# Optimization experiments

Measured on AMD Instinct MI355X. Metric: run time of the kernel, lower is better.

## Reference

```python
import jax, jax.numpy as jnp
import numpy as np
from jax import lax

B, DIM, H, W = 2, 128, 192, 192
GS = [16, 32, 32, 48]          # group ratios [1,2,2,3]/8 of DIM
HID = int(DIM * 2.66)          # 340, Restormer-style hidden width


def _pool_mat(n_in, n_out):
    # torch AdaptiveAvgPool as an explicit linear map [n_out, n_in]
    P = np.zeros((n_out, n_in), np.float32)
    for o in range(n_out):
        s = (o * n_in) // n_out
        e = ((o + 1) * n_in + n_out - 1) // n_out
        P[o, s:e] = 1.0 / (e - s)
    return jnp.asarray(P)


def _ln(t, w, b):
    # WithBias LayerNorm over the channel dim of NCHW (== LN over last dim of b(hw)c)
    mu = t.mean(1, keepdims=True)
    var = ((t - mu) ** 2).mean(1, keepdims=True)
    return (t - mu) / jnp.sqrt(var + 1e-5) * w[None, :, None, None] + b[None, :, None, None]


def _c1x1(t, w):
    return jnp.einsum('oc,bchw->bohw', w, t)


def _dw3(t, w):
    return lax.conv_general_dilated(t, w, (1, 1), 'SAME',
                                    dimension_numbers=('NCHW', 'OIHW', 'NCHW'),
                                    feature_group_count=t.shape[1])


def _c1d(t, w, b):
    return jnp.einsum('oc,bcl->bol', w, t) + b[None, :, None]


def _gelu(t):
    return jax.nn.gelu(t, approximate=False)


def _forward(x, qv_cache, ln1_w, ln1_b, ln2_w, ln2_b, temperature, w_qkv, w_qkv_dw, w_proj,
             intra_down_w, intra_down_b, intra_up_w, intra_up_b, intra_gate_w, intra_gate_b,
             inter0_cw_w, inter0_cw_b, inter0_g_w, inter0_g_b,
             inter1_cw_w, inter1_cw_b, inter1_g_w, inter1_g_b,
             inter2_cw_w, inter2_cw_b, inter2_g_w, inter2_g_b,
             inter3_cw_w, inter3_cw_b, inter3_g_w, inter3_g_b,
             ffn_in_w, ffn_dw_w, ffn_out_w):
    b, c, h, w_ = x.shape
    hw = h * w_
    inter_p = [(inter0_cw_w, inter0_cw_b, inter0_g_w, inter0_g_b),
               (inter1_cw_w, inter1_cw_b, inter1_g_w, inter1_g_b),
               (inter2_cw_w, inter2_cw_b, inter2_g_w, inter2_g_b),
               (inter3_cw_w, inter3_cw_b, inter3_g_w, inter3_g_b)]
    # ---- attention branch ----
    xn = _ln(x, ln1_w, ln1_b)
    qkv = _dw3(_c1x1(xn, w_qkv), w_qkv_dw)
    q, k, v = jnp.split(qkv, 3, axis=1)
    q = q.reshape(b, c, hw); k = k.reshape(b, c, hw); v = v.reshape(b, c, hw)
    # correlation-based channel re-grouping (torch.corrcoef on batch-mean of q)
    cf = q.mean(0)                                   # [C, HW]
    xm = cf - cf.mean(1, keepdims=True)
    cov = xm @ xm.T
    dsd = jnp.sqrt(jnp.diagonal(cov))
    corr = cov / (dsd[:, None] * dsd[None, :])
    idx = jnp.argsort(-corr.mean(1))                 # descending mean similarity
    q = q[:, idx]; k = k[:, idx]; v = v[:, idx]
    atts, tmpc, outs = [], [], []
    start = 0
    for i, g in enumerate(GS):
        qg = q[:, start:start + g]; kg = k[:, start:start + g]; vg = v[:, start:start + g]
        start += g
        qn = qg / jnp.maximum(jnp.linalg.norm(qg, axis=-1, keepdims=True), 1e-12)
        kn = kg / jnp.maximum(jnp.linalg.norm(kg, axis=-1, keepdims=True), 1e-12)
        att = jax.nn.softmax(jnp.einsum('bcl,bdl->bcd', qn, kn) * temperature[i, 0, 0], axis=-1)
        tmpc.append(lax.stop_gradient(qn) + lax.stop_gradient(kn))
        # Inter_CacheModulation: adaptive-pool cache to [g,g], FiLM + gated conv1d
        cw_w, cw_b, g_w, g_b = inter_p[i]
        P = _pool_mat(c, g)
        aligned = jnp.einsum('oi,bij,pj->bop', P, qv_cache, P)    # [1, g, g]
        scale, shift = jnp.split(_c1d(aligned + att, cw_w, cw_b), 2, axis=1)
        x1p = att * scale + shift
        att = x1p * _gelu(_c1d(x1p, g_w, g_b)) + att
        atts.append(att)
        outs.append(jnp.einsum('bcd,bdl->bcl', att, vg))
    # CalculateCurrentLayerCache: resize each group's batch-mean attn to [C,C].
    # Original does (u * c_i) // dim with c_i == dim, i.e. elementwise floor.
    acc = jnp.zeros((1, c, c), x.dtype)
    for a in atts:
        m = lax.stop_gradient(a).mean(0, keepdims=True)[:, None]  # [1,1,g,g]
        u = jax.image.resize(m, (1, 1, c, c), method='bilinear')
        acc = acc + jnp.floor(u)[:, 0]
    qv_new = qv_cache * 0.9 + acc * 0.1
    out_all = jnp.concatenate(outs, axis=1)          # [B, C, HW]
    tmp_all = jnp.concatenate(tmpc, axis=1)
    # Intra_CacheModulation
    s = tmp_all + out_all
    gated = _gelu(_c1d(s, intra_gate_w, intra_gate_b)) * s
    out_all = _c1d(_c1d(gated, intra_down_w, intra_down_b), intra_up_w, intra_up_b) + out_all
    x1 = x + _c1x1(out_all.reshape(b, c, h, w_), w_proj)
    # ---- gated-dconv FFN ----
    xn2 = _ln(x1, ln2_w, ln2_b)
    y1, y2 = jnp.split(_dw3(_c1x1(xn2, ffn_in_w), ffn_dw_w), 2, axis=1)
    out = x1 + _c1x1(_gelu(y1) * y2, ffn_out_w)
    return out, qv_new


def setup_inputs() -> dict:
    key = jax.random.key(0)
    ks = jax.random.split(key, 40)
    def w(i, shape, s=0.02):
        return jax.random.normal(ks[i], shape, jnp.float32) * s
    p = {}
    p['x'] = jax.random.normal(ks[0], (B, DIM, H, W), jnp.float32)
    p['qv_cache'] = jax.random.uniform(ks[1], (1, DIM, DIM), jnp.float32)
    p['ln1_w'] = jnp.ones((DIM,), jnp.float32); p['ln1_b'] = jnp.zeros((DIM,), jnp.float32)
    p['ln2_w'] = jnp.ones((DIM,), jnp.float32); p['ln2_b'] = jnp.zeros((DIM,), jnp.float32)
    p['temperature'] = jnp.ones((4, 1, 1), jnp.float32)
    p['w_qkv'] = w(2, (3 * DIM, DIM))
    p['w_qkv_dw'] = w(3, (3 * DIM, 1, 3, 3))
    p['w_proj'] = w(4, (DIM, DIM))
    p['intra_down_w'] = w(5, (DIM // 2, DIM)); p['intra_down_b'] = jnp.zeros((DIM // 2,), jnp.float32)
    p['intra_up_w'] = w(6, (DIM, DIM // 2)); p['intra_up_b'] = jnp.zeros((DIM,), jnp.float32)
    p['intra_gate_w'] = w(7, (DIM, DIM)); p['intra_gate_b'] = jnp.zeros((DIM,), jnp.float32)
    for i, g in enumerate(GS):
        p[f'inter{i}_cw_w'] = w(8 + 2 * i, (2 * g, g))
        p[f'inter{i}_cw_b'] = jnp.zeros((2 * g,), jnp.float32)
        p[f'inter{i}_g_w'] = w(9 + 2 * i, (g, g))
        p[f'inter{i}_g_b'] = jnp.zeros((g,), jnp.float32)
    p['ffn_in_w'] = w(20, (2 * HID, DIM))
    p['ffn_dw_w'] = w(21, (2 * HID, 1, 3, 3))
    p['ffn_out_w'] = w(22, (DIM, HID))
    return p


def reference(x, qv_cache, ln1_w, ln1_b, ln2_w, ln2_b, temperature, w_qkv, w_qkv_dw, w_proj,
              intra_down_w, intra_down_b, intra_up_w, intra_up_b, intra_gate_w, intra_gate_b,
              inter0_cw_w, inter0_cw_b, inter0_g_w, inter0_g_b,
              inter1_cw_w, inter1_cw_b, inter1_g_w, inter1_g_b,
              inter2_cw_w, inter2_cw_b, inter2_g_w, inter2_g_b,
              inter3_cw_w, inter3_cw_b, inter3_g_w, inter3_g_b,
              ffn_in_w, ffn_dw_w, ffn_out_w):
    return _forward(x, qv_cache, ln1_w, ln1_b, ln2_w, ln2_b, temperature, w_qkv, w_qkv_dw, w_proj,
                    intra_down_w, intra_down_b, intra_up_w, intra_up_b, intra_gate_w, intra_gate_b,
                    inter0_cw_w, inter0_cw_b, inter0_g_w, inter0_g_b,
                    inter1_cw_w, inter1_cw_b, inter1_g_w, inter1_g_b,
                    inter2_cw_w, inter2_cw_b, inter2_g_w, inter2_g_b,
                    inter3_cw_w, inter3_cw_b, inter3_g_w, inter3_g_b,
                    ffn_in_w, ffn_dw_w, ffn_out_w)
```

## Files before the change

### kernel.cpp

```cpp
#include <hip/hip_runtime.h>
#include <math.h>

#define TPB 256

constexpr int BN_  = 2;
constexpr int CDIM = 128;
constexpr int HH   = 192;
constexpr int WW   = 192;
constexpr int HWc  = HH * WW;
constexpr int C3   = 384;
constexpr int HID  = 340;
constexpr int NL2  = 288;
constexpr int CH2  = HWc / NL2;
constexpr int CV   = 288;

typedef unsigned short bf16_t;
typedef __attribute__((ext_vector_type(8))) __bf16 bf16x8;
typedef __attribute__((ext_vector_type(4))) float f32x4;

__device__ __forceinline__ float b2f(bf16_t v) {
  unsigned u = ((unsigned)v) << 16;
  return __uint_as_float(u);
}
__device__ __forceinline__ bf16_t f2b(float f) {
  unsigned u = __float_as_uint(f);
  unsigned r = (u + 0x7FFFu + ((u >> 16) & 1u)) >> 16;
  return (bf16_t)r;
}
__device__ __forceinline__ float ldf(const float* p) { return *p; }
__device__ __forceinline__ float ldf(const bf16_t* p) { return b2f(*p); }
__device__ __forceinline__ void stf(float* p, float v) { *p = v; }
__device__ __forceinline__ void stf(bf16_t* p, float v) { *p = f2b(v); }

__device__ __forceinline__ void ldv4(const float* p, float* v) {
  float4 t = *(const float4*)p;
  v[0] = t.x; v[1] = t.y; v[2] = t.z; v[3] = t.w;
}
__device__ __forceinline__ void ldv4(const bf16_t* p, float* v) {
  ushort4 t = *(const ushort4*)p;
  v[0] = b2f(t.x); v[1] = b2f(t.y); v[2] = b2f(t.z); v[3] = b2f(t.w);
}
__device__ __forceinline__ void stv4(float* p, const float* v) {
  float4 t; t.x = v[0]; t.y = v[1]; t.z = v[2]; t.w = v[3];
  *(float4*)p = t;
}
__device__ __forceinline__ void stv4(bf16_t* p, const float* v) {
  ushort4 t; t.x = f2b(v[0]); t.y = f2b(v[1]); t.z = f2b(v[2]); t.w = f2b(v[3]);
  *(ushort4*)p = t;
}

__device__ __forceinline__ float gelu_f(float x) {
  return 0.5f * x * (1.0f + erff(x * 0.7071067811865475f));
}

__device__ __forceinline__ void unpack8(uint4 v, float* rv) {
  unsigned wv[4] = {v.x, v.y, v.z, v.w};
#pragma unroll
  for (int j = 0; j < 8; ++j)
    rv[j + 1] = b2f((bf16_t)((wv[j >> 1] >> ((j & 1) * 16)) & 0xFFFFu));
}
__device__ __forceinline__ uint4 pack8(const float* a) {
  uint4 o;
  unsigned w[4];
#pragma unroll
  for (int p = 0; p < 4; ++p) {
    unsigned lo = f2b(a[2 * p]), hi = f2b(a[2 * p + 1]);
    w[p] = lo | (hi << 16);
  }
  o.x = w[0]; o.y = w[1]; o.z = w[2]; o.w = w[3];
  return o;
}
__device__ __forceinline__ float sumsq8(uint4 v) {
  unsigned w[4] = {v.x, v.y, v.z, v.w};
  float s = 0.f;
#pragma unroll
  for (int j = 0; j < 8; ++j) {
    float t = b2f((bf16_t)((w[j >> 1] >> ((j & 1) * 16)) & 0xFFFFu));
    s += t * t;
  }
  return s;
}

__device__ __forceinline__ void dwrow(const bf16_t* rp, int w8, float* rv) {
  unpack8(*(const uint4*)rp, rv);
  rv[0] = (w8 > 0) ? b2f(rp[-1]) : 0.f;
  rv[9] = (w8 + 8 < WW) ? b2f(rp[8]) : 0.f;
}

__device__ __constant__ int dGSZ[4]   = {16, 32, 32, 48};
__device__ __constant__ int dGST[4]   = {0, 16, 48, 80};
__device__ __constant__ int dAOFF[4]  = {0, 256, 1280, 2304};
__device__ __constant__ int dABASE[4] = {0, 512, 2560, 4608};

constexpr size_t oATTRAW  = 0;
constexpr size_t oATTS2   = 65536;
constexpr size_t oWB      = 131072;
constexpr size_t oQKP2    = 602112;
constexpr size_t oMUPC    = 897024;
constexpr size_t oATTS    = 1327104;
constexpr size_t oNORMQ   = 1363968;
constexpr size_t oNORMK   = 1364992;
constexpr size_t oIDX     = 1366016;
constexpr size_t oMU      = 1366528;
constexpr size_t oCOV     = 1367040;
constexpr size_t oQKV     = 1572864;
constexpr size_t oXN      = 58195968;
constexpr size_t oOUTALL  = 77070336;
constexpr size_t oSBUF    = 95944704;
constexpr size_t WS_NEED  = 114819072;
constexpr size_t oCHUNK1  = oOUTALL;
constexpr size_t oCOVPART = oOUTALL;
constexpr size_t oCOVP2   = oSBUF;
constexpr size_t oQKPART  = oXN;
constexpr size_t oGATED   = oQKV;
constexpr size_t oDBUF    = oQKV + 18874368;
constexpr size_t oY0C     = oOUTALL;
constexpr size_t oZ       = oQKV;
constexpr size_t oX1B     = oXN;

constexpr int eWQ   = 0;
constexpr int eGATE = 49152;
constexpr int eDOWN = 65536;
constexpr int eUP   = 73728;
constexpr int ePROJ = 81920;
constexpr int eFFI  = 98304;
constexpr int eFFO  = 185344;
constexpr int eTOT  = 234496;

__global__ __launch_bounds__(TPB) void k_wcvt(const float* __restrict__ wq,
                                              const float* __restrict__ gate,
                                              const float* __restrict__ down,
                                              const float* __restrict__ up,
                                              const float* __restrict__ proj,
                                              const float* __restrict__ ffi,
                                              const float* __restrict__ ffo,
                                              bf16_t* __restrict__ wb) {
  int t = blockIdx.x * TPB + threadIdx.x;
  if (t >= eTOT) return;
  int u = t;
  if (u < 49152) { wb[eWQ + u] = f2b(wq[u]); return; }
  u -= 49152;
  if (u < 16384) { wb[eGATE + u] = f2b(gate[u]); return; }
  u -= 16384;
  if (u < 8192)  { wb[eDOWN + u] = f2b(down[u]); return; }
  u -= 8192;
  if (u < 8192)  { wb[eUP + u] = f2b(up[u]); return; }
  u -= 8192;
  if (u < 16384) { wb[ePROJ + u] = f2b(proj[u]); return; }
  u -= 16384;
  if (u < 87040) { wb[eFFI + u] = f2b(ffi[u]); return; }
  u -= 87040;
  {
    int o = u / 384, k = u - o * 384;
    wb[eFFO + u] = (k < HID) ? f2b(ffo[o * HID + k]) : (bf16_t)0;
  }
}

template <typename TI>
__global__ __launch_bounds__(TPB) void k_ln(const TI* __restrict__ x,
                                            const float* __restrict__ w,
                                            const float* __restrict__ bias,
                                            bf16_t* __restrict__ out) {
  int t = blockIdx.x * TPB + threadIdx.x;
  if (t >= BN_ * HWc) return;
  int b = t / HWc, l = t - b * HWc;
  const TI* xb = x + (size_t)b * CDIM * HWc + l;
  float s = 0.f, s2 = 0.f;
#pragma unroll 4
  for (int c = 0; c < CDIM; ++c) { float v = ldf(&xb[(size_t)c * HWc]); s += v; s2 += v * v; }
  float mu  = s * (1.f / CDIM);
  float var = s2 * (1.f / CDIM) - mu * mu;
  float inv = 1.f / sqrtf(var + 1e-5f);
  bf16_t* ob = out + (size_t)b * CDIM * HWc + l;
#pragma unroll 4
  for (int c = 0; c < CDIM; ++c)
    stf(&ob[(size_t)c * HWc], (ldf(&xb[(size_t)c * HWc]) - mu) * inv * w[c] + bias[c]);
}

template <typename TO, typename TA, int KT, int EPI>
__global__ __launch_bounds__(TPB) void k_mgA(const bf16_t* __restrict__ W,
                                             const bf16_t* __restrict__ W2, int osplit,
                                             const float* __restrict__ bias,
                                             const bf16_t* __restrict__ in,
                                             const TA* __restrict__ aux,
                                             TO* __restrict__ out, int O,
                                             int ibr, int obr, int abr) {
  constexpr int L  = HWc;
  constexpr int PK = KT + 8;
  constexpr int KH = KT / 2;
  constexpr int SH = (KT == 128) ? 6 : 5;
  __shared__ bf16_t At[128 * PK];
  __shared__ bf16_t Wt[64 * PK];
  int b = blockIdx.y;
  const bf16_t* inb  = in  + (size_t)b * ibr * L;
  const TA*     auxb = aux ? aux + (size_t)b * abr * L : nullptr;
  TO*           outb = out + (size_t)b * obr * L;
  int l0 = blockIdx.x * 128;
  int tid = threadIdx.x, lane = tid & 63, wid = tid >> 6;
// ... 104 lines not shown
  const TA*     auxb = aux ? aux + (size_t)b * abr * L : nullptr;
  TO*           outb = out + (size_t)b * obr * L;
  int l0 = blockIdx.x * 128;
  int tid = threadIdx.x, lane = tid & 63, wid = tid >> 6;
  int wm = wid >> 1, wn = wid & 1;
  int cl = lane & 15, rg = lane >> 4;

  f32x4 acc[4][4];
#pragma unroll
  for (int m = 0; m < 4; ++m)
#pragma unroll
    for (int n = 0; n < 4; ++n) acc[m][n] = (f32x4){0.f, 0.f, 0.f, 0.f};

  for (int k0 = 0; k0 < K; k0 += BK) {
#pragma unroll
    for (int r = 0; r < 2; ++r) {
      int u = tid + r * TPB;
      int k2 = u & 31, lb = u >> 5;
      int ka = k0 + k2 * 2;
      uint4 rowA = {0u,0u,0u,0u}, rowB = {0u,0u,0u,0u};
      if (ka < K)     rowA = *(const uint4*)(&inb[(size_t)ka * L + l0 + lb * 8]);
      if (ka + 1 < K) rowB = *(const uint4*)(&inb[(size_t)(ka + 1) * L + l0 + lb * 8]);
      unsigned wa[4] = {rowA.x, rowA.y, rowA.z, rowA.w};
      unsigned wb[4] = {rowB.x, rowB.y, rowB.z, rowB.w};
#pragma unroll
      for (int j = 0; j < 8; ++j) {
        unsigned va = (wa[j >> 1] >> ((j & 1) * 16)) & 0xFFFFu;
        unsigned vb = (wb[j >> 1] >> ((j & 1) * 16)) & 0xFFFFu;
        *(unsigned*)(&At[(lb * 8 + j) * PK + k2 * 2]) = va | (vb << 16);
      }
    }
#pragma unroll
    for (int r = 0; r < 4; ++r) {
      int e = tid + r * TPB;
      int o = e >> 3, k8 = (e & 7) * 8;
      uint4 wv = *(const uint4*)(&Wb[(size_t)o * WSTR + k0 + k8]);
      *(uint4*)(&Wt[o * PK + k8]) = wv;
    }
    __syncthreads();
#pragma unroll
    for (int kk = 0; kk < 2; ++kk) {
      int kof = kk * 32 + rg * 8;
      bf16x8 a[4], bfr[4];
#pragma unroll
      for (int m = 0; m < 4; ++m)
        a[m] = *(const bf16x8*)(&Wt[(wm * 64 + m * 16 + cl) * PK + kof]);
#pragma unroll
      for (int n = 0; n < 4; ++n)
        bfr[n] = *(const bf16x8*)(&At[(wn * 64 + n * 16 + cl) * PK + kof]);
#pragma unroll
      for (int m = 0; m < 4; ++m)
#pragma unroll
        for (int n = 0; n < 4; ++n)
          acc[m][n] = __builtin_amdgcn_mfma_f32_16x16x32_bf16(bfr[n], a[m], acc[m][n], 0, 0, 0);
    }
    __syncthreads();
  }
#pragma unroll
  for (int m = 0; m < 4; ++m) {
    int og = wm * 64 + m * 16 + cl;
    if (og >= O) continue;
    float bv = bias ? bias[og] : 0.f;
#pragma unroll
    for (int n = 0; n < 4; ++n) {
      int lcol = l0 + wn * 64 + n * 16 + rg * 4;
      size_t off = (size_t)og * L + lcol;
      float v[4];
#pragma unroll
      for (int r = 0; r < 4; ++r) v[r] = acc[m][n][r] + bv;
      if (EPI == 1) {
        float a4[4]; ldv4(&auxb[off], a4);
#pragma unroll
        for (int r = 0; r < 4; ++r) v[r] += a4[r];
      } else if (EPI == 2) {
        float a4[4]; ldv4(&auxb[off], a4);
#pragma unroll
        for (int r = 0; r < 4; ++r) v[r] = gelu_f(v[r]) * a4[r];
      }
      stv4(&outb[off], v);
    }
  }
}

__global__ __launch_bounds__(TPB) void k_dw3v(const bf16_t* __restrict__ in,
                                              const float* __restrict__ wt,
                                              bf16_t* __restrict__ out,
                                              int Cc, int c0, int CoutTotal, long totalG) {
  long t = (long)blockIdx.x * TPB + threadIdx.x;
  if (t >= totalG) return;
  int g = (int)(t % (HWc / 16));
  long bc = t / (HWc / 16);
  int cl = (int)(bc % Cc);
  int b = (int)(bc / Cc);
  int rp = g / (WW / 8), w8 = (g % (WW / 8)) * 8;
  int h = rp * 2;
  const bf16_t* ib = in + ((size_t)b * Cc + cl) * HWc;
  const float* wc = wt + (size_t)(c0 + cl) * 9;
  float rv[4][10];
#pragma unroll
  for (int dy = 0; dy < 4; ++dy) {
    int hh = h - 1 + dy;
    if (hh < 0 || hh >= HH) {
#pragma unroll
      for (int j = 0; j < 10; ++j) rv[dy][j] = 0.f;
    } else {
      dwrow(ib + hh * WW + w8, w8, rv[dy]);
    }
  }
  float a0[8], a1[8];
#pragma unroll
  for (int j = 0; j < 8; ++j) {
    float s0 = 0.f, s1 = 0.f;
#pragma unroll
    for (int dy = 0; dy < 3; ++dy)
#pragma unroll
      for (int dx = 0; dx < 3; ++dx) {
        float wv = wc[dy * 3 + dx];
        s0 += rv[dy][j + dx] * wv;
        s1 += rv[dy + 1][j + dx] * wv;
      }
    a0[j] = s0; a1[j] = s1;
  }
  bf16_t* ob = out + ((size_t)b * CoutTotal + c0 + cl) * HWc + h * WW + w8;
  *(uint4*)ob = pack8(a0);
  *(uint4*)(ob + WW) = pack8(a1);
}

__global__ __launch_bounds__(TPB) void k_cov4(const bf16_t* __restrict__ qkv,
                                              float* __restrict__ part,
                                              float* __restrict__ mupartC) {
  constexpr int PK = 136;
  __shared__ bf16_t Xt[128 * PK];
  int chunk = blockIdx.x;
  int base = chunk * 128;
  int tid = threadIdx.x, lane = tid & 63, wid = tid >> 6;
  int wm = wid >> 1, wn = wid & 1;
  int cl = lane & 15, rg = lane >> 4;
#pragma unroll
  for (int r = 0; r < 8; ++r) {
    int u = tid + r * TPB;
    int c = u >> 4, l8 = (u & 15) * 8;
    uint4 v0 = *(const uint4*)(&qkv[(size_t)c * HWc + base + l8]);
    uint4 v1 = *(const uint4*)(&qkv[(size_t)C3 * HWc + (size_t)c * HWc + base + l8]);
    unsigned w0[4] = {v0.x, v0.y, v0.z, v0.w};
    unsigned w1[4] = {v1.x, v1.y, v1.z, v1.w};
    float cf[8];
#pragma unroll
    for (int j = 0; j < 8; ++j) {
      float a = b2f((bf16_t)((w0[j >> 1] >> ((j & 1) * 16)) & 0xFFFFu));
      float bq = b2f((bf16_t)((w1[j >> 1] >> ((j & 1) * 16)) & 0xFFFFu));
      cf[j] = 0.5f * (a + bq);
    }
    *(uint4*)(&Xt[c * PK + l8]) = pack8(cf);
  }
  __syncthreads();
  {
    int c = tid >> 1, half = tid & 1;
    float s = 0.f;
    for (int l = half * 64; l < half * 64 + 64; ++l)
      s += b2f(Xt[c * PK + l]);
    s += __shfl_xor(s, 1, 64);
    if (half == 0) mupartC[(size_t)chunk * CDIM + c] = s;
  }
  f32x4 acc[4][4];
#pragma unroll
  for (int m = 0; m < 4; ++m)
// ... 107 lines not shown
  }
}

template <int G>
__device__ __forceinline__ void qk2_impl(char* sm, const bf16_t* __restrict__ qkv,
                                         const int* __restrict__ idx, int start,
                                         float* __restrict__ partial, int nl, int b) {
  constexpr int RT = G / 16;
  constexpr int U  = G * CH2 / 8;
  float (*qs)[CH2 + 2] = (float (*)[CH2 + 2])sm;
  float (*ks)[CH2 + 2] = (float (*)[CH2 + 2])(sm + (size_t)G * (CH2 + 2) * 4);
  int* idxg = (int*)(sm + (size_t)2 * G * (CH2 + 2) * 4);
  int tid = threadIdx.x;
  if (tid < G) idxg[tid] = idx[start + tid];
  __syncthreads();
  int l0 = nl * CH2;
  for (int u = tid; u < U; u += TPB) {
    int r = u / (CH2 / 8), c8 = (u % (CH2 / 8)) * 8;
    int ch = idxg[r];
    uint4 vq = *(const uint4*)(&qkv[((size_t)b * C3 + ch) * HWc + l0 + c8]);
    uint4 vk = *(const uint4*)(&qkv[((size_t)b * C3 + CDIM + ch) * HWc + l0 + c8]);
    unsigned wq[4] = {vq.x, vq.y, vq.z, vq.w};
    unsigned wk[4] = {vk.x, vk.y, vk.z, vk.w};
#pragma unroll
    for (int j = 0; j < 8; ++j) {
      qs[r][c8 + j] = b2f((bf16_t)((wq[j >> 1] >> ((j & 1) * 16)) & 0xFFFFu));
      ks[r][c8 + j] = b2f((bf16_t)((wk[j >> 1] >> ((j & 1) * 16)) & 0xFFFFu));
    }
  }
  __syncthreads();
  int ti = tid & 15, tj = tid >> 4;
  float acc[RT][RT];
#pragma unroll
  for (int m = 0; m < RT; ++m)
#pragma unroll
    for (int n = 0; n < RT; ++n) acc[m][n] = 0.f;
#pragma unroll 4
  for (int l = 0; l < CH2; ++l) {
    float qa[RT], kb[RT];
#pragma unroll
    for (int m = 0; m < RT; ++m) qa[m] = qs[ti * RT + m][l];
#pragma unroll
    for (int n = 0; n < RT; ++n) kb[n] = ks[tj * RT + n][l];
#pragma unroll
    for (int m = 0; m < RT; ++m)
#pragma unroll
      for (int n = 0; n < RT; ++n) acc[m][n] += qa[m] * kb[n];
  }
  float* pb = partial + ((size_t)(b * NL2) + nl) * G * G;
#pragma unroll
  for (int m = 0; m < RT; ++m)
#pragma unroll
    for (int n = 0; n < RT; ++n)
      pb[(ti * RT + m) * G + tj * RT + n] = acc[m][n];
}

__global__ __launch_bounds__(TPB) void k_qk2g(const bf16_t* __restrict__ qkv,
                                              const int* __restrict__ idx,
                                              float* __restrict__ qkpart) {
  extern __shared__ char sm[];
  int nl = blockIdx.x, b = blockIdx.y, gi = blockIdx.z;
  if (gi == 0)      qk2_impl<16>(sm, qkv, idx, 0,  qkpart + 0,       nl, b);
  else if (gi == 1) qk2_impl<32>(sm, qkv, idx, 16, qkpart + 147456,  nl, b);
  else if (gi == 2) qk2_impl<32>(sm, qkv, idx, 48, qkpart + 737280,  nl, b);
  else              qk2_impl<48>(sm, qkv, idx, 80, qkpart + 1327104, nl, b);
}

__global__ __launch_bounds__(TPB) void k_qkred1(const float* __restrict__ qkpart,
                                                float* __restrict__ qkp2) {
  int t = blockIdx.x * TPB + threadIdx.x;
  int yg = blockIdx.y;
  int b = t / 4608, e = t - b * 4608;
  int gi = (e < 256) ? 0 : (e < 1280) ? 1 : (e < 2304) ? 2 : 3;
  const int gg4[4]    = {256, 1024, 1024, 2304};
  const int pgoff[4]  = {0, 147456, 737280, 1327104};
  const int aoff4[4]  = {0, 256, 1280, 2304};
  int GGg = gg4[gi];
  int el = e - aoff4[gi];
  const float* pb = qkpart + pgoff[gi] + (size_t)(b * NL2) * GGg + el;
  float s = 0.f;
  for (int nl = yg * 36; nl < (yg + 1) * 36; ++nl) s += pb[(size_t)nl * GGg];
  qkp2[(size_t)yg * (BN_ * 4608) + t] = s;
}
__global__ __launch_bounds__(TPB) void k_qkred2(const float* __restrict__ qkp2,
                                                float* __restrict__ attraw) {
  int t = blockIdx.x * TPB + threadIdx.x;
  if (t >= BN_ * 4608) return;
  float s = 0.f;
#pragma unroll
  for (int y = 0; y < 8; ++y) s += qkp2[(size_t)y * (BN_ * 4608) + t];
  attraw[t] = s;
}

__global__ __launch_bounds__(TPB) void k_smg(const float* __restrict__ attraw,
                                             const int* __restrict__ idx,
                                             const float* __restrict__ invq,
                                             const float* __restrict__ invk,
                                             const float* __restrict__ temperature,
                                             float* __restrict__ attS) {
  int b = blockIdx.x, gi = blockIdx.y;
  int G = dGSZ[gi], start = dGST[gi];
  int GG = G * G;
  const float* ar = attraw + b * 4608 + dAOFF[gi];
  float* as = attS + b * 4608 + dAOFF[gi];
  float temp = temperature[gi];
  __shared__ float att[2304];
  __shared__ float ivq[48], ivk[48];
  int tid = threadIdx.x;
  if (tid < G) {
    int ch = idx[start + tid];
    ivq[tid] = invq[b * CDIM + ch];
    ivk[tid] = invk[b * CDIM + ch];
  }
  __syncthreads();
  for (int e = tid; e < GG; e += TPB) {
    int i = e / G, j = e - i * G;
    att[e] = ar[e] * temp * ivq[i] * ivk[j];
  }
  __syncthreads();
  if (tid < G) {
    float mx = -3.4e38f;
    for (int j = 0; j < G; ++j) mx = fmaxf(mx, att[tid * G + j]);
    float ssum = 0.f;
    for (int j = 0; j < G; ++j) { float ex = expf(att[tid * G + j] - mx); att[tid * G + j] = ex; ssum += ex; }
    float inv = 1.f / ssum;
    for (int j = 0; j < G; ++j) att[tid * G + j] *= inv;
  }
  __syncthreads();
  for (int e = tid; e < GG; e += TPB) as[e] = att[e];
}

__global__ __launch_bounds__(TPB) void k_imlpg(const float* __restrict__ attS,
                                               const float* __restrict__ qv_cache,
                                               const float* __restrict__ cw0, const float* __restrict__ cb0,
                                               const float* __restrict__ gw0, const float* __restrict__ gb0,
                                               const float* __restrict__ cw1, const float* __restrict__ cb1,
                                               const float* __restrict__ gw1, const float* __restrict__ gb1,
                                               const float* __restrict__ cw2, const float* __restrict__ cb2,
                                               const float* __restrict__ gw2, const float* __restrict__ gb2,
                                               const float* __restrict__ cw3, const float* __restrict__ cb3,
                                               const float* __restrict__ gw3, const float* __restrict__ gb3,
                                               float* __restrict__ attF) {
  int b = blockIdx.x, gi = blockIdx.y, tile = blockIdx.z;
  int G = dGSZ[gi];
  int p0 = tile * 16;
  if (p0 >= G) return;
  int GG = G * G;
  const float* cw_w = (gi == 0) ? cw0 : (gi == 1) ? cw1 : (gi == 2) ? cw2 : cw3;
  const float* cw_b = (gi == 0) ? cb0 : (gi == 1) ? cb1 : (gi == 2) ? cb2 : cb3;
  const float* g_w  = (gi == 0) ? gw0 : (gi == 1) ? gw1 : (gi == 2) ? gw2 : gw3;
  const float* g_b  = (gi == 0) ? gb0 : (gi == 1) ? gb1 : (gi == 2) ? gb2 : gb3;
  const float* as = attS + b * 4608 + dAOFF[gi];
  float* af = attF + dABASE[gi] + (size_t)b * GG;
  int tid = threadIdx.x;
  __shared__ float cwW[2 * 48 * 48];
  __shared__ float gW[48 * 48];
  __shared__ float attC[48 * 16], t1C[48 * 16], scC[48 * 16], shC[48 * 16],
                   x1pC[48 * 16], t2C[48 * 16];
  for (int e = tid; e < 2 * G * G; e += TPB) cwW[e] = cw_w[e];
  for (int e = tid; e < G * G; e += TPB) gW[e] = g_w[e];
  for (int u = tid; u < G * 16; u += TPB) {
    int c = u >> 4, pl = u & 15;
    int p = p0 + pl;
    float av = 0.f, pv = 0.f;
    if (p < G) {
      av = as[c * G + p];
      int so = c * CDIM / G, eo = ((c + 1) * CDIM + G - 1) / G;
      int sp = p * CDIM / G, ep = ((p + 1) * CDIM + G - 1) / G;
      float ssum = 0.f;
      for (int i2 = so; i2 < eo; ++i2)
        for (int j2 = sp; j2 < ep; ++j2) ssum += qv_cache[i2 * CDIM + j2];
      pv = ssum / (float)((eo - so) * (ep - sp));
    }
    attC[u] = av;
    t1C[u] = pv + av;
  }
  __syncthreads();
  for (int u = tid; u < 2 * G * 16; u += TPB) {
    int o = u >> 4, pl = u & 15;
    float acc = cw_b[o];
    for (int c = 0; c < G; ++c) acc += cwW[o * G + c] * t1C[c * 16 + pl];
    if (o < G) scC[o * 16 + pl] = acc;
    else       shC[(o - G) * 16 + pl] = acc;
  }
  __syncthreads();
  for (int u = tid; u < G * 16; u += TPB)
    x1pC[u] = attC[u] * scC[u] + shC[u];
  __syncthreads();
  for (int u = tid; u < G * 16; u += TPB) {
    int o = u >> 4, pl = u & 15;
    float acc = g_b[o];
    for (int c = 0; c < G; ++c) acc += gW[o * G + c] * x1pC[c * 16 + pl];
    t2C[u] = acc;
  }
  __syncthreads();
  for (int u = tid; u < G * 16; u += TPB) {
    int c = u >> 4, pl = u & 15;
    int p = p0 + pl;
    if (p < G)
      af[c * G + p] = x1pC[u] * gelu_f(t2C[u]) + attC[u];
// ... 149 lines not shown
#pragma unroll
  for (int dy = 0; dy < 4; ++dy) {
    int hh = h - 1 + dy;
    if (hh < 0 || hh >= HH) {
#pragma unroll
      for (int j = 0; j < 10; ++j) rv[dy][j] = 0.f;
    } else {
      dwrow(i1 + hh * WW + w8, w8, rv[dy]);
    }
  }
  float g0[8], g1[8];
#pragma unroll
  for (int j = 0; j < 8; ++j) {
    float s0 = 0.f, s1 = 0.f;
#pragma unroll
    for (int dy = 0; dy < 3; ++dy)
#pragma unroll
      for (int dx = 0; dx < 3; ++dx) {
        float wv = w1[dy * 3 + dx];
        s0 += rv[dy][j + dx] * wv;
        s1 += rv[dy + 1][j + dx] * wv;
      }
    g0[j] = gelu_f(s0); g1[j] = gelu_f(s1);
  }
#pragma unroll
  for (int dy = 0; dy < 4; ++dy) {
    int hh = h - 1 + dy;
    if (hh < 0 || hh >= HH) {
#pragma unroll
      for (int j = 0; j < 10; ++j) rv[dy][j] = 0.f;
    } else {
      dwrow(i2 + hh * WW + w8, w8, rv[dy]);
    }
  }
  float o0[8], o1[8];
#pragma unroll
  for (int j = 0; j < 8; ++j) {
    float s0 = 0.f, s1 = 0.f;
#pragma unroll
    for (int dy = 0; dy < 3; ++dy)
#pragma unroll
      for (int dx = 0; dx < 3; ++dx) {
        float wv = w2[dy * 3 + dx];
        s0 += rv[dy][j + dx] * wv;
        s1 += rv[dy + 1][j + dx] * wv;
      }
    o0[j] = g0[j] * s0; o1[j] = g1[j] * s1;
  }
  bf16_t* zp = z + ((size_t)b * HID + c0 + cl) * HWc + h * WW + w8;
  *(uint4*)zp = pack8(o0);
  *(uint4*)(zp + WW) = pack8(o1);
}

extern "C" void kernel_launch(void* const* d_in, const int* in_sizes, int n_in,
                              void* d_out, int out_size, void* d_ws, size_t ws_size,
                              hipStream_t stream) {
  if (ws_size < WS_NEED) return;

  const float* x        = (const float*)d_in[0];
  const float* qv_cache = (const float*)d_in[1];
  const float* ln1_w    = (const float*)d_in[2];
  const float* ln1_b    = (const float*)d_in[3];
  const float* ln2_w    = (const float*)d_in[4];
  const float* ln2_b    = (const float*)d_in[5];
  const float* temperature = (const float*)d_in[6];
  const float* w_qkv    = (const float*)d_in[7];
  const float* w_qkv_dw = (const float*)d_in[8];
  const float* w_proj   = (const float*)d_in[9];
  const float* intra_down_w = (const float*)d_in[10];
  const float* intra_down_b = (const float*)d_in[11];
  const float* intra_up_w   = (const float*)d_in[12];
  const float* intra_up_b   = (const float*)d_in[13];
  const float* intra_gate_w = (const float*)d_in[14];
  const float* intra_gate_b = (const float*)d_in[15];
  const float* ffn_in_w  = (const float*)d_in[32];
  const float* ffn_dw_w  = (const float*)d_in[33];
  const float* ffn_out_w = (const float*)d_in[34];

  char* wsb = (char*)d_ws;
  float* out    = (float*)d_out;
  float* out_qv = out + (size_t)BN_ * CDIM * HWc;
  bf16_t* xn2   = (bf16_t*)d_out;

  float*  attraw  = (float*)(wsb + oATTRAW);
  float*  attS    = (float*)(wsb + oATTS2);
  bf16_t* wb      = (bf16_t*)(wsb + oWB);
  float*  qkp2    = (float*)(wsb + oQKP2);
  float*  mupartC = (float*)(wsb + oMUPC);
  float*  atts    = (float*)(wsb + oATTS);
  float*  invqA   = (float*)(wsb + oNORMQ);
  float*  invkA   = (float*)(wsb + oNORMK);
  int*    idx     = (int*)(wsb + oIDX);
  float*  mu      = (float*)(wsb + oMU);
  float*  cov     = (float*)(wsb + oCOV);
  bf16_t* qkv     = (bf16_t*)(wsb + oQKV);
  bf16_t* xn      = (bf16_t*)(wsb + oXN);
  bf16_t* out_all = (bf16_t*)(wsb + oOUTALL);
  bf16_t* sbuf    = (bf16_t*)(wsb + oSBUF);
  bf16_t* chunk1  = (bf16_t*)(wsb + oCHUNK1);
  float*  covpart = (float*)(wsb + oCOVPART);
  float*  covp2   = (float*)(wsb + oCOVP2);
  float*  qkpart  = (float*)(wsb + oQKPART);
  bf16_t* gated   = (bf16_t*)(wsb + oGATED);
  bf16_t* dbuf    = (bf16_t*)(wsb + oDBUF);
  bf16_t* x1b     = (bf16_t*)(wsb + oX1B);
  bf16_t* y0c     = (bf16_t*)(wsb + oY0C);
  bf16_t* zbuf    = (bf16_t*)(wsb + oZ);

  const bf16_t* wq_b   = wb + eWQ;
  const bf16_t* gate_b = wb + eGATE;
  const bf16_t* down_b = wb + eDOWN;
  const bf16_t* up_b   = wb + eUP;
  const bf16_t* proj_b = wb + ePROJ;
  const bf16_t* ffi_b  = wb + eFFI;
  const bf16_t* ffo_b  = wb + eFFO;

  const int GX = HWc / 128;
  const int NOS = 1 << 30;
  dim3 gA(GX, BN_);

  k_wcvt<<<(eTOT + TPB - 1) / TPB, TPB, 0, stream>>>(
      w_qkv, intra_gate_w, intra_down_w, intra_up_w, w_proj, ffn_in_w, ffn_out_w, wb);

  k_ln<float><<<(BN_ * HWc + TPB - 1) / TPB, TPB, 0, stream>>>(x, ln1_w, ln1_b, xn);

  for (int ci = 0; ci < 2; ++ci) {
    int c0 = ci * 192;
    k_mgA<bf16_t, float, 128, 0><<<gA, TPB, 0, stream>>>(
        wq_b + (size_t)c0 * CDIM, wq_b, NOS, nullptr, xn, nullptr, chunk1,
        192, CDIM, 192, 0);
    long totG = (long)BN_ * 192 * (HWc / 16);
    k_dw3v<<<(unsigned)((totG + TPB - 1) / TPB), TPB, 0, stream>>>(
        chunk1, w_qkv_dw, qkv, 192, c0, C3, totG);
  }

  k_norms<<<dim3(CDIM, BN_, 2), TPB, 0, stream>>>(qkv, invqA, invkA);

  k_cov4<<<CV, TPB, 0, stream>>>(qkv, covpart, mupartC);
  k_muredC<<<CDIM, TPB, 0, stream>>>(mupartC, mu);
  k_covred1<<<dim3(64, 8), TPB, 0, stream>>>(covpart, covp2);
  k_covred2<<<64, TPB, 0, stream>>>(covp2, mu, cov);
  k_rank<<<1, CDIM, 0, stream>>>(cov, idx);

  {
    size_t dyn = (size_t)2 * 48 * (CH2 + 2) * 4 + 48 * 4;
    k_qk2g<<<dim3(NL2, BN_, 4), TPB, dyn, stream>>>(qkv, idx, qkpart);
  }
  k_qkred1<<<dim3(36, 8), TPB, 0, stream>>>(qkpart, qkp2);
  k_qkred2<<<36, TPB, 0, stream>>>(qkp2, attraw);
  k_smg<<<dim3(BN_, 4), TPB, 0, stream>>>(attraw, idx, invqA, invkA, temperature, attS);
  k_imlpg<<<dim3(BN_, 4, 3), TPB, 0, stream>>>(
      attS, qv_cache,
      (const float*)d_in[16], (const float*)d_in[17], (const float*)d_in[18], (const float*)d_in[19],
      (const float*)d_in[20], (const float*)d_in[21], (const float*)d_in[22], (const float*)d_in[23],
      (const float*)d_in[24], (const float*)d_in[25], (const float*)d_in[26], (const float*)d_in[27],
      (const float*)d_in[28], (const float*)d_in[29], (const float*)d_in[30], (const float*)d_in[31],
      atts);
  {
    size_t dyn = (size_t)128 * 72 * 2 + (size_t)48 * 72 * 2 + 48 * 4;
    k_avg<<<dim3(HWc / 128, BN_, 4), TPB, dyn, stream>>>(
        qkv, idx, atts, invqA, invkA, out_all, sbuf);
  }
  k_qvnew<<<(CDIM * CDIM + TPB - 1) / TPB, TPB, 0, stream>>>(atts, qv_cache, out_qv);

  k_mgA<bf16_t, float, 128, 3><<<gA, TPB, 0, stream>>>(
      gate_b, gate_b, NOS, intra_gate_b, sbuf, nullptr, gated,
      CDIM, CDIM, CDIM, 0);
  k_mgA<bf16_t, float, 128, 0><<<gA, TPB, 0, stream>>>(
      down_b, down_b, NOS, intra_down_b, gated, nullptr, dbuf,
      CDIM / 2, CDIM, CDIM / 2, 0);
  k_mgA<bf16_t, bf16_t, 64, 1><<<gA, TPB, 0, stream>>>(
      up_b, up_b, NOS, intra_up_b, dbuf, out_all, out_all,
      CDIM, CDIM / 2, CDIM, CDIM);
  k_mgA<bf16_t, float, 128, 1><<<gA, TPB, 0, stream>>>(
      proj_b, proj_b, NOS, nullptr, out_all, x, x1b, CDIM, CDIM, CDIM, CDIM);
  k_ln<bf16_t><<<(BN_ * HWc + TPB - 1) / TPB, TPB, 0, stream>>>(x1b, ln2_w, ln2_b, xn2);

  const int fcc[3] = {114, 114, 112};
  const int fc0[3] = {0, 114, 228};
  for (int ci = 0; ci < 3; ++ci) {
    int Cc = fcc[ci], c0 = fc0[ci];
    k_mgA<bf16_t, float, 128, 0><<<gA, TPB, 0, stream>>>(
        ffi_b + (size_t)c0 * CDIM, ffi_b + (size_t)(HID + c0) * CDIM, Cc,
        nullptr, xn2, nullptr, y0c, 2 * Cc, CDIM, 2 * Cc, 0);
    long totG = (long)BN_ * Cc * (HWc / 16);
    k_dwgeluv<<<(unsigned)((totG + TPB - 1) / TPB), TPB, 0, stream>>>(
        y0c, ffn_dw_w, zbuf, Cc, c0, totG);
  }
  k_mgB<float, bf16_t, 1><<<gA, TPB, 0, stream>>>(
      ffo_b, nullptr, zbuf, x1b, out, CDIM, HID, HID, CDIM, CDIM);
}
```

Before: 513.5 us.

## Fuse gate/down/up/proj GEMM chain into one LDS-resident kernel; fold qkred2 into softmax

Replaces four separate GEMM launches (gated intra-MLP gate, down, up with residual, and output projection with skip) with one kernel that keeps each 128-column activation tile in shared memory across all four stages. Only the weights are restaged per stage, so the gated, dbuf and out_all intermediates no longer round-trip through global memory. Separately, the final 8-way partial sum of the attention logits is folded into the softmax kernel, removing a tiny launch. The fused kernel needs about 103 KB of dynamic LDS, which limits occupancy to roughly one block per CU, and it adds many barriers between stages.

```diff
diff --git a/kernel.cpp b/kernel.cpp
--- a/kernel.cpp
+++ b/kernel.cpp
@@ -92,7 +92,6 @@
 __device__ __constant__ int dAOFF[4]  = {0, 256, 1280, 2304};
 __device__ __constant__ int dABASE[4] = {0, 512, 2560, 4608};
 
-constexpr size_t oATTRAW  = 0;
 constexpr size_t oATTS2   = 65536;
 constexpr size_t oWB      = 131072;
 constexpr size_t oQKP2    = 602112;
@@ -112,8 +111,6 @@
 constexpr size_t oCOVPART = oOUTALL;
 constexpr size_t oCOVP2   = oSBUF;
 constexpr size_t oQKPART  = oXN;
-constexpr size_t oGATED   = oQKV;
-constexpr size_t oDBUF    = oQKV + 18874368;
 constexpr size_t oY0C     = oOUTALL;
 constexpr size_t oZ       = oQKV;
 constexpr size_t oX1B     = oXN;
@@ -384,6 +381,177 @@
   }
 }
 
+template <int KT>
+__device__ __forceinline__ void stage_w64(bf16_t* Wt, const bf16_t* Wsrc, int tid) {
+  constexpr int PKl = KT + 8;
+#pragma unroll
+  for (int r = 0; r < (64 * KT / 8) / TPB; ++r) {
+    int e = tid + r * TPB;
+    int o = e / (KT / 8), k8 = (e % (KT / 8)) * 8;
+    *(uint4*)(&Wt[o * PKl + k8]) = *(const uint4*)(&Wsrc[(size_t)o * KT + k8]);
+  }
+}
+
+template <int KT>
+__device__ __forceinline__ void gemm_tile(const bf16_t* Wt, const bf16_t* Ain,
+                                          int wm, int wn, int cl, int rg,
+                                          f32x4 acc[2][4]) {
+  constexpr int PKl = KT + 8;
+#pragma unroll
+  for (int m = 0; m < 2; ++m)
+#pragma unroll
+    for (int n = 0; n < 4; ++n) acc[m][n] = (f32x4){0.f, 0.f, 0.f, 0.f};
+#pragma unroll
+  for (int kk = 0; kk < KT / 32; ++kk) {
+    int kof = kk * 32 + rg * 8;
+    bf16x8 a[2], bb[4];
+#pragma unroll
+    for (int m = 0; m < 2; ++m)
+      a[m] = *(const bf16x8*)(&Wt[(wm * 32 + m * 16 + cl) * PKl + kof]);
+#pragma unroll
+    for (int n = 0; n < 4; ++n)
+      bb[n] = *(const bf16x8*)(&Ain[(wn * 64 + n * 16 + cl) * PKl + kof]);
+#pragma unroll
+    for (int m = 0; m < 2; ++m)
+#pragma unroll
+      for (int n = 0; n < 4; ++n)
+        acc[m][n] = __builtin_amdgcn_mfma_f32_16x16x32_bf16(bb[n], a[m], acc[m][n], 0, 0, 0);
+  }
+}
+
+__global__ __launch_bounds__(TPB) void k_mlp4(const bf16_t* __restrict__ wbarena,
+                                              const float* __restrict__ gb,
+                                              const float* __restrict__ db,
+                                              const float* __restrict__ ub,
+                                              const bf16_t* __restrict__ sbuf,
+                                              const bf16_t* __restrict__ out_all,
+                                              const float* __restrict__ x,
+                                              bf16_t* __restrict__ x1b) {
+  constexpr int L = HWc;
+  constexpr int PK = 136;
+  constexpr int PK3 = 72;
+  extern __shared__ char sm[];
+  bf16_t* As = (bf16_t*)sm;
+  bf16_t* Ag = (bf16_t*)(sm + 34816);
+  bf16_t* Ad = (bf16_t*)(sm + 69632);
+  bf16_t* Wt = (bf16_t*)(sm + 88064);
+  bf16_t* Ao = As;
+  int b = blockIdx.y;
+  int l0 = blockIdx.x * 128;
+  int tid = threadIdx.x, lane = tid & 63, wid = tid >> 6;
+  int wm = wid >> 1, wn = wid & 1;
+  int cl = lane & 15, rg = lane >> 4;
+  const bf16_t* inb = sbuf + (size_t)b * CDIM * L;
+
+#pragma unroll
+  for (int r = 0; r < 4; ++r) {
+    int u = tid + r * TPB;
+    int k2 = u & 63, lb = u >> 6;
+    int ka = k2 * 2;
+    uint4 rowA = *(const uint4*)(&inb[(size_t)ka * L + l0 + lb * 8]);
+    uint4 rowB = *(const uint4*)(&inb[(size_t)(ka + 1) * L + l0 + lb * 8]);
+    unsigned wa[4] = {rowA.x, rowA.y, rowA.z, rowA.w};
+    unsigned wbv[4] = {rowB.x, rowB.y, rowB.z, rowB.w};
+#pragma unroll
+    for (int j = 0; j < 8; ++j) {
+      unsigned va = (wa[j >> 1] >> ((j & 1) * 16)) & 0xFFFFu;
+      unsigned vb = (wbv[j >> 1] >> ((j & 1) * 16)) & 0xFFFFu;
+      *(unsigned*)(&As[(lb * 8 + j) * PK + ka]) = va | (vb << 16);
+    }
+  }
+
+  for (int oc = 0; oc < 2; ++oc) {
+    stage_w64<128>(Wt, wbarena + eGATE + (size_t)(oc * 64) * 128, tid);
+    __syncthreads();
+    f32x4 acc[2][4];
+    gemm_tile<128>(Wt, As, wm, wn, cl, rg, acc);
+    __syncthreads();
+#pragma unroll
+    for (int m = 0; m < 2; ++m) {
+      int og = oc * 64 + wm * 32 + m * 16 + cl;
+      float bv = gb[og];
+#pragma unroll
+      for (int n = 0; n < 4; ++n) {
+        int lloc = wn * 64 + n * 16 + rg * 4;
+#pragma unroll
+        for (int r = 0; r < 4; ++r) {
+          float v = gelu_f(acc[m][n][r] + bv) * b2f(As[(lloc + r) * PK + og]);
+          Ag[(lloc + r) * PK + og] = f2b(v);
+        }
+      }
+    }
+    __syncthreads();
+  }
+
+  stage_w64<128>(Wt, wbarena + eDOWN, tid);
+  __syncthreads();
+  {
+    f32x4 acc[2][4];
+    gemm_tile<128>(Wt, Ag, wm, wn, cl, rg, acc);
+    __syncthreads();
+#pragma unroll
+    for (int m = 0; m < 2; ++m) {
+      int og = wm * 32 + m * 16 + cl;
+      float bv = db[og];
+#pragma unroll
+      for (int n = 0; n < 4; ++n) {
+        int lloc = wn * 64 + n * 16 + rg * 4;
+#pragma unroll
+        for (int r = 0; r < 4; ++r)
+          Ad[(lloc + r) * PK3 + og] = f2b(acc[m][n][r] + bv);
+      }
+    }
+    __syncthreads();
+  }
+
+  const bf16_t* oab = out_all + (size_t)b * CDIM * L;
+  for (int oc = 0; oc < 2; ++oc) {
+    stage_w64<64>(Wt, wbarena + eUP + (size_t)(oc * 64) * 64, tid);
+    __syncthreads();
+    f32x4 acc[2][4];
+    gemm_tile<64>((const bf16_t*)Wt, Ad, wm, wn, cl, rg, acc);
+    __syncthreads();
+#pragma unroll
+    for (int m = 0; m < 2; ++m) {
+      int og = oc * 64 + wm * 32 + m * 16 + cl;
+      float bv = ub[og];
+#pragma unroll
+      for (int n = 0; n < 4; ++n) {
+        int lloc = wn * 64 + n * 16 + rg * 4;
+        float a4[4]; ldv4(&oab[(size_t)og * L + l0 + lloc], a4);
+#pragma unroll
+        for (int r = 0; r < 4; ++r)
+          Ao[(lloc + r) * PK + og] = f2b(acc[m][n][r] + bv + a4[r]);
+      }
+    }
+    __syncthreads();
+  }
+
+  const float* xb = x + (size_t)b * CDIM * L;
+  bf16_t* x1bb = x1b + (size_t)b * CDIM * L;
+  for (int oc = 0; oc < 2; ++oc) {
+    stage_w64<128>(Wt, wbarena + ePROJ + (size_t)(oc * 64) * 128, tid);
+    __syncthreads();
+    f32x4 acc[2][4];
+    gemm_tile<128>(Wt, Ao, wm, wn, cl, rg, acc);
+    __syncthreads();
+#pragma unroll
+    for (int m = 0; m < 2; ++m) {
+      int og = oc * 64 + wm * 32 + m * 16 + cl;
+#pragma unroll
+      for (int n = 0; n < 4; ++n) {
+        int lcol = l0 + wn * 64 + n * 16 + rg * 4;
+        size_t off = (size_t)og * L + lcol;
+        float v[4], a4[4];
+        ldv4(&xb[off], a4);
+#pragma unroll
+        for (int r = 0; r < 4; ++r) v[r] = acc[m][n][r] + a4[r];
+        stv4(&x1bb[off], v);
+      }
+    }
+  }
+}
+
 __global__ __launch_bounds__(TPB) void k_dw3v(const bf16_t* __restrict__ in,
                                               const float* __restrict__ wt,
                                               bf16_t* __restrict__ out,
@@ -657,17 +825,8 @@
   for (int nl = yg * 36; nl < (yg + 1) * 36; ++nl) s += pb[(size_t)nl * GGg];
   qkp2[(size_t)yg * (BN_ * 4608) + t] = s;
 }
-__global__ __launch_bounds__(TPB) void k_qkred2(const float* __restrict__ qkp2,
-                                                float* __restrict__ attraw) {
-  int t = blockIdx.x * TPB + threadIdx.x;
-  if (t >= BN_ * 4608) return;
-  float s = 0.f;
-#pragma unroll
-  for (int y = 0; y < 8; ++y) s += qkp2[(size_t)y * (BN_ * 4608) + t];
-  attraw[t] = s;
-}
-
-__global__ __launch_bounds__(TPB) void k_smg(const float* __restrict__ attraw,
+
+__global__ __launch_bounds__(TPB) void k_smg(const float* __restrict__ qkp2,
                                              const int* __restrict__ idx,
                                              const float* __restrict__ invq,
                                              const float* __restrict__ invk,
@@ -676,7 +835,6 @@
   int b = blockIdx.x, gi = blockIdx.y;
   int G = dGSZ[gi], start = dGST[gi];
   int GG = G * G;
-  const float* ar = attraw + b * 4608 + dAOFF[gi];
   float* as = attS + b * 4608 + dAOFF[gi];
   float temp = temperature[gi];
   __shared__ float att[2304];
@@ -689,8 +847,12 @@
   }
   __syncthreads();
   for (int e = tid; e < GG; e += TPB) {
+    int base = b * 4608 + dAOFF[gi] + e;
+    float s = 0.f;
+#pragma unroll
+    for (int y = 0; y < 8; ++y) s += qkp2[(size_t)y * (BN_ * 4608) + base];
     int i = e / G, j = e - i * G;
-    att[e] = ar[e] * temp * ivq[i] * ivk[j];
+    att[e] = s * temp * ivq[i] * ivk[j];
   }
   __syncthreads();
   if (tid < G) {
@@ -1006,7 +1168,6 @@
   float* out_qv = out + (size_t)BN_ * CDIM * HWc;
   bf16_t* xn2   = (bf16_t*)d_out;
 
-  float*  attraw  = (float*)(wsb + oATTRAW);
   float*  attS    = (float*)(wsb + oATTS2);
   bf16_t* wb      = (bf16_t*)(wsb + oWB);
   float*  qkp2    = (float*)(wsb + oQKP2);
@@ -1025,23 +1186,24 @@
   float*  covpart = (float*)(wsb + oCOVPART);
   float*  covp2   = (float*)(wsb + oCOVP2);
   float*  qkpart  = (float*)(wsb + oQKPART);
-  bf16_t* gated   = (bf16_t*)(wsb + oGATED);
-  bf16_t* dbuf    = (bf16_t*)(wsb + oDBUF);
   bf16_t* x1b     = (bf16_t*)(wsb + oX1B);
   bf16_t* y0c     = (bf16_t*)(wsb + oY0C);
   bf16_t* zbuf    = (bf16_t*)(wsb + oZ);
 
   const bf16_t* wq_b   = wb + eWQ;
-  const bf16_t* gate_b = wb + eGATE;
-  const bf16_t* down_b = wb + eDOWN;
-  const bf16_t* up_b   = wb + eUP;
-  const bf16_t* proj_b = wb + ePROJ;
   const bf16_t* ffi_b  = wb + eFFI;
   const bf16_t* ffo_b  = wb + eFFO;
 
   const int GX = HWc / 128;
   const int NOS = 1 << 30;
   dim3 gA(GX, BN_);
+
+  static bool s_attr = false;
+  if (!s_attr) {
+    hipFuncSetAttribute((const void*)k_mlp4,
+                        hipFuncAttributeMaxDynamicSharedMemorySize, 105472);
+    s_attr = true;
+  }
 
   k_wcvt<<<(eTOT + TPB - 1) / TPB, TPB, 0, stream>>>(
       w_qkv, intra_gate_w, intra_down_w, intra_up_w, w_proj, ffn_in_w, ffn_out_w, wb);
@@ -1071,8 +1233,7 @@
     k_qk2g<<<dim3(NL2, BN_, 4), TPB, dyn, stream>>>(qkv, idx, qkpart);
   }
   k_qkred1<<<dim3(36, 8), TPB, 0, stream>>>(qkpart, qkp2);
-  k_qkred2<<<36, TPB, 0, stream>>>(qkp2, attraw);
-  k_smg<<<dim3(BN_, 4), TPB, 0, stream>>>(attraw, idx, invqA, invkA, temperature, attS);
+  k_smg<<<dim3(BN_, 4), TPB, 0, stream>>>(qkp2, idx, invqA, invkA, temperature, attS);
   k_imlpg<<<dim3(BN_, 4, 3), TPB, 0, stream>>>(
       attS, qv_cache,
       (const float*)d_in[16], (const float*)d_in[17], (const float*)d_in[18], (const float*)d_in[19],
@@ -1087,17 +1248,9 @@
   }
   k_qvnew<<<(CDIM * CDIM + TPB - 1) / TPB, TPB, 0, stream>>>(atts, qv_cache, out_qv);
 
-  k_mgA<bf16_t, float, 128, 3><<<gA, TPB, 0, stream>>>(
-      gate_b, gate_b, NOS, intra_gate_b, sbuf, nullptr, gated,
-      CDIM, CDIM, CDIM, 0);
-  k_mgA<bf16_t, float, 128, 0><<<gA, TPB, 0, stream>>>(
-      down_b, down_b, NOS, intra_down_b, gated, nullptr, dbuf,
-      CDIM / 2, CDIM, CDIM / 2, 0);
-  k_mgA<bf16_t, bf16_t, 64, 1><<<gA, TPB, 0, stream>>>(
-      up_b, up_b, NOS, intra_up_b, dbuf, out_all, out_all,
-      CDIM, CDIM / 2, CDIM, CDIM);
-  k_mgA<bf16_t, float, 128, 1><<<gA, TPB, 0, stream>>>(
-      proj_b, proj_b, NOS, nullptr, out_all, x, x1b, CDIM, CDIM, CDIM, CDIM);
+  k_mlp4<<<gA, TPB, 105472, stream>>>(
+      wb, intra_gate_b, intra_down_b, intra_up_b, sbuf, out_all, x, x1b);
+
   k_ln<bf16_t><<<(BN_ * HWc + TPB - 1) / TPB, TPB, 0, stream>>>(x1b, ln2_w, ln2_b, xn2);
 
   const int fcc[3] = {114, 114, 112};
```

Result: slower. 526.0 us (+2.4%).
